# Kernel tuning notes

Hardware: AMD Instinct MI355X
Metric: run time of the kernel (lower is better)

The kernel has to match this reference:

```python
import jax, jax.numpy as jnp
import numpy as np

B, H, S, DH = 1, 16, 4096, 64
SPARSITY = 0.1
NEG = -1e9


def setup_inputs() -> dict:
    key = jax.random.key(0)
    kq, kk, kv, kp, km = jax.random.split(key, 5)
    query = jax.random.normal(kq, (B, H, S, DH), dtype=jnp.float32)
    k_ = jax.random.normal(kk, (B, H, S, DH), dtype=jnp.float32)
    v_ = jax.random.normal(kv, (B, H, S, DH), dtype=jnp.float32)
    pat = jax.random.uniform(kp, (S, S)) < SPARSITY
    pat = pat | jnp.eye(S, dtype=bool)
    sparse_pattern = pat[None, None]  # [1,1,S,S]
    mask = jax.random.randint(km, (1, 1, 1, S), 0, 2, dtype=jnp.int32)
    return {"query": query, "key": k_, "value": v_,
            "sparse_pattern": sparse_pattern, "mask": mask}


def reference(query, key, value, sparse_pattern, mask):
    scale = 1.0 / jnp.sqrt(jnp.asarray(DH, dtype=query.dtype))
    # [B,H,S,S] attention scores
    scores = jnp.einsum('bhqd,bhkd->bhqk', query, key) * scale
    scores = jnp.where(sparse_pattern, scores, NEG)
    scores = jnp.where(mask == 0, NEG, scores)
    weights = jax.nn.softmax(scores, axis=-1)
    return jnp.einsum('bhqk,bhkd->bhqd', weights, value)
```

## Files before the change

### kernel.cpp

```cpp
#include <hip/hip_runtime.h>
#include <hip/hip_bf16.h>

#define S_LEN 4096
#define DHD   64
#define NH    16
#define NKT   64
#define KVB   64
#define WQ    32
#define NW    4
#define QB    (WQ * NW)
#define QSCALE 0.18033688011112042f
#define THRS   8.656170245333781f

#if __has_builtin(__builtin_amdgcn_exp2f)
#define EXP2(x) __builtin_amdgcn_exp2f(x)
#else
#define EXP2(x) exp2f(x)
#endif

typedef __bf16 bf16x8 __attribute__((ext_vector_type(8)));
typedef __bf16 bf16x4 __attribute__((ext_vector_type(4)));
typedef float  f32x16 __attribute__((ext_vector_type(16)));
typedef float  f32x4  __attribute__((ext_vector_type(4)));
typedef unsigned u32;
typedef unsigned u32x4v __attribute__((ext_vector_type(4)));
typedef unsigned long long u64;

__device__ __forceinline__ int swz(int row, int col) {
  return row * 64 + ((((col >> 3) ^ (row & 7)) << 3) | (col & 7));
}

__device__ __forceinline__ u32 pk(float a, float b) {
  __bf16 x = (__bf16)a, y = (__bf16)b;
  u32 lo = (u32)__builtin_bit_cast(unsigned short, x);
  u32 hi = (u32)__builtin_bit_cast(unsigned short, y);
  return lo | (hi << 16);
}

__device__ __forceinline__ void gload16(const void* g, void* l) {
  __builtin_amdgcn_global_load_lds((const __attribute__((address_space(1))) void*)g,
                                   (__attribute__((address_space(3))) void*)l, 16, 0, 0);
}

union PAW { u32x4v w; bf16x8 h; };

template <int MODE>
__device__ __forceinline__ bool patget(const void* __restrict__ p, int q, int k) {
  const size_t idx = (size_t)q * S_LEN + k;
  if constexpr (MODE == 1) return ((const unsigned char*)p)[idx] != 0;
  else if constexpr (MODE == 0) return ((const int*)p)[idx] != 0;
  else return ((const float*)p)[idx] != 0.0f;
}

__global__ void __launch_bounds__(256, 2) attn32c(
    const float* __restrict__ Qg, const __bf16* __restrict__ Kc, const __bf16* __restrict__ Vc,
    const u64* __restrict__ packw,
    const int* __restrict__ cntp, float* __restrict__ out) {
  __shared__ __align__(16) __bf16 Kls[2][KVB * DHD];
  __shared__ __align__(16) __bf16 Vls[2][DHD * KVB];
  __shared__ float sfb[NW][WQ];

  const int gid = (blockIdx.x & 7) * 64 + (blockIdx.x >> 3);
  const int h = gid >> 5;
  const int q0 = (gid & 31) * QB;

  const int t = threadIdx.x, lane = t & 63, wv = t >> 6;
  const int l32 = lane & 31, hi = lane >> 5;
  const int qrow = q0 + wv * WQ + l32;
  const int nact = cntp[0];
  const int nt = (nact + 63) >> 6;

  bf16x8 aQ[4];
  {
    const float* qp = Qg + ((size_t)h * S_LEN + qrow) * DHD;
#pragma unroll
    for (int c = 0; c < 4; c++) {
      float4 x = *(const float4*)(qp + c * 16 + hi * 8);
      float4 y = *(const float4*)(qp + c * 16 + hi * 8 + 4);
      bf16x8 f;
      f[0] = (__bf16)(x.x * QSCALE); f[1] = (__bf16)(x.y * QSCALE);
      f[2] = (__bf16)(x.z * QSCALE); f[3] = (__bf16)(x.w * QSCALE);
      f[4] = (__bf16)(y.x * QSCALE); f[5] = (__bf16)(y.y * QSCALE);
      f[6] = (__bf16)(y.z * QSCALE); f[7] = (__bf16)(y.w * QSCALE);
      aQ[c] = f;
    }
  }
  bf16x8 onesf;
#pragma unroll
  for (int j = 0; j < 8; j++) onesf[j] = (__bf16)1.0f;

  const __bf16* Kb = Kc + (size_t)h * NKT * 4096;
  const __bf16* Vb = Vc + (size_t)h * NKT * 4096;

  auto stage = [&](int buf, int kt) {
    const __bf16* kbase = Kb + (size_t)kt * 4096;
    const __bf16* vbase = Vb + (size_t)kt * 4096;
#pragma unroll
    for (int i = 0; i < 2; i++) {
      const int j = wv * 2 + i;
      gload16(kbase + j * 512 + lane * 8, &Kls[buf][j * 512]);
      gload16(vbase + j * 512 + lane * 8, &Vls[buf][j * 512]);
    }
  };

  f32x16 Oc0, Oc1, Ol;
#pragma unroll
  for (int r = 0; r < 16; r++) { Oc0[r] = 0.f; Oc1[r] = 0.f; Ol[r] = 0.f; }
  float m_run = -__builtin_inff();
  const u64* prow = packw + qrow;

  stage(0, 0);
  __syncthreads();
  int cur = 0;

  for (int kt = 0; kt < nt; kt++) {
    if (kt + 1 < nt) stage(cur ^ 1, kt + 1);

    const u64 pw = prow[(size_t)kt * S_LEN];

    const __bf16* Kl = Kls[cur];
    f32x16 p0, p1;
#pragma unroll
    for (int r = 0; r < 16; r++) { p0[r] = 0.f; p1[r] = 0.f; }
    __builtin_amdgcn_s_setprio(1);
#pragma unroll
    for (int c = 0; c < 4; c++) {
      const int g = (((2 * c + hi) ^ (l32 & 7)) << 3);
      const bf16x8 k0 = *(const bf16x8*)&Kl[l32 * 64 + g];
      const bf16x8 k1 = *(const bf16x8*)&Kl[(32 + l32) * 64 + g];
      p0 = __builtin_amdgcn_mfma_f32_32x32x16_bf16(k0, aQ[c], p0, 0, 0, 0);
      p1 = __builtin_amdgcn_mfma_f32_32x32x16_bf16(k1, aQ[c], p1, 0, 0, 0);
    }
    __builtin_amdgcn_s_setprio(0);

    float mx[16];
#pragma unroll
    for (int i = 0; i < 8; i++) mx[i] = fmaxf(p0[2 * i], p0[2 * i + 1]);
#pragma unroll
    for (int i = 0; i < 8; i++) mx[8 + i] = fmaxf(p1[2 * i], p1[2 * i + 1]);
#pragma unroll
    for (int s = 8; s >= 1; s >>= 1)
#pragma unroll
      for (int i = 0; i < s; i++) mx[i] = fmaxf(mx[i], mx[i + s]);
    const float pm = fmaxf(mx[0], __shfl_xor(mx[0], 32));

    if (!__all(pm <= m_run + THRS)) {
      const float mn = fmaxf(m_run, pm);
      const float sf = EXP2(m_run - mn);
      m_run = mn;
      if (lane < 32) sfb[wv][l32] = sf;
#pragma unroll
      for (int rq = 0; rq < 4; rq++) {
        const f32x4 s4 = *(const f32x4*)&sfb[wv][rq * 8 + 4 * hi];
#pragma unroll
        for (int rr = 0; rr < 4; rr++) {
          Oc0[rq * 4 + rr] *= s4[rr];
          Oc1[rq * 4 + rr] *= s4[rr];
          Ol[rq * 4 + rr]  *= s4[rr];
        }
      }
    }

    const u32 b0 = (u32)pw, b1 = (u32)(pw >> 32);
    const u32 w0 = hi ? ((b0 >> 4) | (b1 << 28)) : b0;
    const u32 w1 = hi ? (b1 >> 4) : b1;

#pragma unroll
    for (int r = 0; r < 16; r++) {
      const int sp = (r & 3) + 8 * (r >> 2);
      float e0 = EXP2(p0[r] - m_run);
      float e1 = EXP2(p1[r] - m_run);
      const int t0 = (int)(w0 << (31 - sp)) >> 31;
      const int t1 = (int)(w1 << (31 - sp)) >> 31;
      p0[r] = __uint_as_float(__float_as_uint(e0) & (u32)t0);
      p1[r] = __uint_as_float(__float_as_uint(e1) & (u32)t1);
    }

    const __bf16* Vl = Vls[cur];
    __builtin_amdgcn_s_setprio(1);
#pragma unroll
    for (int ks = 0; ks < 4; ks++) {
      const f32x16& ps = (ks < 2) ? p0 : p1;
      const int b = (ks & 1) * 8;
      const u32 a0 = pk(ps[b + 0], ps[b + 1]), a1 = pk(ps[b + 2], ps[b + 3]);
      const u32 c0 = pk(ps[b + 4], ps[b + 5]), c1 = pk(ps[b + 6], ps[b + 7]);
      const u32 sa0 = (u32)__shfl_xor((int)a0, 32), sa1 = (u32)__shfl_xor((int)a1, 32);
      const u32 sc0 = (u32)__shfl_xor((int)c0, 32), sc1 = (u32)__shfl_xor((int)c1, 32);
      PAW pa;
      pa.w = (u32x4v){hi ? sc0 : a0, hi ? sc1 : a1, hi ? c0 : sa0, hi ? c1 : sa1};
      const int g = (((2 * ks + hi) ^ (l32 & 7)) << 3);
      const bf16x8 v0 = *(const bf16x8*)&Vl[l32 * 64 + g];
      const bf16x8 v1 = *(const bf16x8*)&Vl[(32 + l32) * 64 + g];
      Oc0 = __builtin_amdgcn_mfma_f32_32x32x16_bf16(pa.h, v0, Oc0, 0, 0, 0);
      Oc1 = __builtin_amdgcn_mfma_f32_32x32x16_bf16(pa.h, v1, Oc1, 0, 0, 0);
      Ol  = __builtin_amdgcn_mfma_f32_32x32x16_bf16(pa.h, onesf, Ol, 0, 0, 0);
    }
    __builtin_amdgcn_s_setprio(0);

    __syncthreads();
    cur ^= 1;
  }

  float* ob = out + ((size_t)h * S_LEN + q0 + wv * WQ) * DHD;
#pragma unroll
  for (int rq = 0; rq < 4; rq++) {
#pragma unroll
    for (int rr = 0; rr < 4; rr++) {
      const int r = rq * 4 + rr;
      const float linv = 1.0f / Ol[r];
      const int qq = rr + 8 * rq + 4 * hi;
      ob[(size_t)qq * DHD + l32]      = Oc0[r] * linv;
      ob[(size_t)qq * DHD + 32 + l32] = Oc1[r] * linv;
    }
  }
}

__global__ void prep0(const unsigned* __restrict__ p, int* __restrict__ flag,
                      const int* __restrict__ mask, int* __restrict__ idx,
                      int* __restrict__ cntp) {
  if (blockIdx.x == 0) {
    __shared__ unsigned red[256];
    const int t = threadIdx.x;
    unsigned acc = 0;
    for (int i = t; i < 16384; i += 256) {
      const unsigned w = p[i];
      if (w == 0x3F800000u) acc |= 2u;
      else if (w & 0xFFFFFF00u) acc |= 1u;
    }
    red[t] = acc;
    __syncthreads();
    if (t == 0) {
      unsigned a = 0;
      for (int i = 0; i < 256; i++) a |= red[i];
      flag[0] = (a & 2u) ? 2 : ((a & 1u) ? 1 : 0);
    }
  } else if (threadIdx.x < 64) {
    const int t = threadIdx.x;
    int cnt = 0;
    for (int j = 0; j < 64; j++) cnt += (mask[t * 64 + j] != 0);
    int inc = cnt;
    for (int d = 1; d < 64; d <<= 1) {
      const int v = __shfl_up(inc, d);
      if (t >= d) inc += v;
    }
    int pfx = inc - cnt;
    for (int j = 0; j < 64; j++) {
      const int k = t * 64 + j;
      if (mask[k] != 0) idx[pfx++] = k;
    }
    if (t == 63) cntp[0] = inc;
  }
}

__global__ void __launch_bounds__(256) pack_compact(
    const void* __restrict__ pat, const int* __restrict__ flagp,
    const int* __restrict__ idx, const int* __restrict__ cntp, u64* __restrict__ packw) {
  __shared__ __align__(16) unsigned rowbuf[4096];
  const int q = blockIdx.x, t = threadIdx.x;
  const int nact = cntp[0];
  const int mode = flagp[0];
  if (mode == 1) {
    const uint4* src = (const uint4*)((const unsigned char*)pat + ((size_t)q << 12));
    ((uint4*)rowbuf)[t] = src[t];
  } else {
    const uint4* src = (const uint4*)((const unsigned*)pat + ((size_t)q << 12));
#pragma unroll
    for (int i = 0; i < 4; i++) ((uint4*)rowbuf)[t + 256 * i] = src[t + 256 * i];
  }
  __syncthreads();
  const unsigned char* rb = (const unsigned char*)rowbuf;
  for (int base = 0; base < nact; base += 256) {
    const int j = base + t;
    bool pb = false;
    if (j < nact) {
      const int k = idx[j];
      pb = (mode == 1) ? (rb[k] != 0) : (rowbuf[k] != 0);
    }
    const u64 b = __ballot(pb);
    if ((t & 63) == 0) packw[(size_t)(j >> 6) * S_LEN + q] = b;
  }
}

__global__ void compact_kv(const float* __restrict__ K, const float* __restrict__ V,
                           const int* __restrict__ idx, const int* __restrict__ cntp,
                           __bf16* __restrict__ Kc, __bf16* __restrict__ Vc) {
  const int kt = blockIdx.x, h = blockIdx.y, t = threadIdx.x;
  const int nact = cntp[0];
  if (kt >= ((nact + 63) >> 6)) return;
  __bf16* Kd = Kc + ((size_t)(h * NKT + kt)) * 4096;
  __bf16* Vd = Vc + ((size_t)(h * NKT + kt)) * 4096;
  const float* Kb = K + (size_t)h * S_LEN * DHD;
  const float* Vb = V + (size_t)h * S_LEN * DHD;
#pragma unroll
  for (int i = 0; i < 4; i++) {
    const int u = t + 256 * i;
    const int kk = u >> 4, d = (u & 15) * 4;
    const int kg = kt * 64 + kk;
    float4 v = {0.f, 0.f, 0.f, 0.f};
    if (kg < nact) v = *(const float4*)(Kb + (size_t)idx[kg] * DHD + d);
    bf16x4 b;
    b[0] = (__bf16)v.x; b[1] = (__bf16)v.y; b[2] = (__bf16)v.z; b[3] = (__bf16)v.w;
    *(bf16x4*)&Kd[swz(kk, d)] = b;
  }
#pragma unroll
  for (int i = 0; i < 2; i++) {
    const int u = t + 256 * i;
    const int kp = u & 31, d4 = u >> 5;
    const int g0 = kt * 64 + 2 * kp, g1 = g0 + 1;
    float4 a = {0.f, 0.f, 0.f, 0.f}, b = {0.f, 0.f, 0.f, 0.f};
    if (g0 < nact) a = *(const float4*)(Vb + (size_t)idx[g0] * DHD + d4 * 4);
    if (g1 < nact) b = *(const float4*)(Vb + (size_t)idx[g1] * DHD + d4 * 4);
    const float* A = reinterpret_cast<const float*>(&a);
    const float* B = reinterpret_cast<const float*>(&b);
#pragma unroll
    for (int j = 0; j < 4; j++) {
      *(u32*)&Vd[swz(d4 * 4 + j, 2 * kp)] = pk(A[j], B[j]);
    }
  }
}

template <bool PACKED, int MODE>
__global__ void __launch_bounds__(256, 2) attn32(
    const float* __restrict__ Qg, const float* __restrict__ Kg, const float* __restrict__ Vg,
    const u64* __restrict__ packw, const void* __restrict__ pat, const int* __restrict__ mask,
    float* __restrict__ out) {
  __shared__ __align__(16) __bf16 Kls[2][KVB * DHD];
  __shared__ __align__(16) __bf16 Vls[2][DHD * KVB];
  __shared__ float sfb[NW][WQ];
  const int gid = (blockIdx.x & 7) * 64 + (blockIdx.x >> 3);
  const int h = gid >> 5;
  const int q0 = (gid & 31) * QB;
  const int t = threadIdx.x, lane = t & 63, wv = t >> 6;
  const int l32 = lane & 31, hi = lane >> 5;
  const int qrow = q0 + wv * WQ + l32;
  bf16x8 aQ[4];
  {
    const float* qp = Qg + ((size_t)h * S_LEN + qrow) * DHD;
#pragma unroll
    for (int c = 0; c < 4; c++) {
      float4 x = *(const float4*)(qp + c * 16 + hi * 8);
      float4 y = *(const float4*)(qp + c * 16 + hi * 8 + 4);
      bf16x8 f;
      f[0] = (__bf16)(x.x * QSCALE); f[1] = (__bf16)(x.y * QSCALE);
      f[2] = (__bf16)(x.z * QSCALE); f[3] = (__bf16)(x.w * QSCALE);
      f[4] = (__bf16)(y.x * QSCALE); f[5] = (__bf16)(y.y * QSCALE);
      f[6] = (__bf16)(y.z * QSCALE); f[7] = (__bf16)(y.w * QSCALE);
      aQ[c] = f;
    }
  }
  const float* Kb = Kg + (size_t)h * S_LEN * DHD;
  const float* Vb = Vg + (size_t)h * S_LEN * DHD;
  float4 kreg[4], vreg0[2], vreg1[2];
  auto issue_loads = [&](int kt) {
    const float* kbase = Kb + (size_t)kt * KVB * DHD;
    const float* vbase = Vb + (size_t)kt * KVB * DHD;
#pragma unroll
    for (int i = 0; i < 4; i++) {
      const int u = t + 256 * i;
      kreg[i] = *(const float4*)(kbase + (size_t)(u >> 4) * DHD + (u & 15) * 4);
    }
#pragma unroll
    for (int i = 0; i < 2; i++) {
      const int u = t + 256 * i;
      const int kp = u & 31, d4 = u >> 5;
      vreg0[i] = *(const float4*)(vbase + (size_t)(2 * kp) * DHD + d4 * 4);
      vreg1[i] = *(const float4*)(vbase + (size_t)(2 * kp + 1) * DHD + d4 * 4);
    }
  };
  auto write_tile = [&](int buf) {
    __bf16* Kd = Kls[buf];
    __bf16* Vd = Vls[buf];
#pragma unroll
    for (int i = 0; i < 4; i++) {
      const int u = t + 256 * i;
      const int kk = u >> 4, d = (u & 15) * 4;
      const float4 v = kreg[i];
      bf16x4 b;
      b[0] = (__bf16)v.x; b[1] = (__bf16)v.y; b[2] = (__bf16)v.z; b[3] = (__bf16)v.w;
      *(bf16x4*)&Kd[swz(kk, d)] = b;
    }
#pragma unroll
    for (int i = 0; i < 2; i++) {
      const int u = t + 256 * i;
      const int kp = u & 31, d4 = u >> 5;
      const float* A = reinterpret_cast<const float*>(&vreg0[i]);
      const float* B = reinterpret_cast<const float*>(&vreg1[i]);
#pragma unroll
      for (int j = 0; j < 4; j++) {
        *(u32*)&Vd[swz(d4 * 4 + j, 2 * kp)] = pk(A[j], B[j]);
      }
    }
  };
  f32x16 Oc0, Oc1;
#pragma unroll
  for (int r = 0; r < 16; r++) { Oc0[r] = 0.f; Oc1[r] = 0.f; }
  float m_run = -__builtin_inff(), l_run = 0.f;
  const u64* prow = PACKED ? (packw + qrow) : nullptr;
  issue_loads(0);
  write_tile(0);
  __syncthreads();
  int cur = 0;
  for (int kt = 0; kt < NKT; kt++) {
    if (kt + 1 < NKT) issue_loads(kt + 1);
    u64 pw;
    if constexpr (PACKED) {
      pw = prow[(size_t)kt * S_LEN];
    } else {
      pw = 0;
      for (int j = 0; j < 64; j++) {
        const bool pb = patget<MODE>(pat, qrow, kt * 64 + j) && (mask[kt * 64 + j] != 0);
        pw |= (u64)pb << j;
      }
    }
    const __bf16* Kl = Kls[cur];
    f32x16 p0, p1;
#pragma unroll
    for (int r = 0; r < 16; r++) { p0[r] = 0.f; p1[r] = 0.f; }
#pragma unroll
    for (int c = 0; c < 4; c++) {
      const int g = (((2 * c + hi) ^ (l32 & 7)) << 3);
      const bf16x8 k0 = *(const bf16x8*)&Kl[l32 * 64 + g];
      const bf16x8 k1 = *(const bf16x8*)&Kl[(32 + l32) * 64 + g];
      p0 = __builtin_amdgcn_mfma_f32_32x32x16_bf16(k0, aQ[c], p0, 0, 0, 0);
      p1 = __builtin_amdgcn_mfma_f32_32x32x16_bf16(k1, aQ[c], p1, 0, 0, 0);
    }
    float pm = p0[0];
#pragma unroll
    for (int r = 1; r < 16; r++) pm = fmaxf(pm, p0[r]);
#pragma unroll
    for (int r = 0; r < 16; r++) pm = fmaxf(pm, p1[r]);
    pm = fmaxf(pm, __shfl_xor(pm, 32));
    if (!__all(pm <= m_run + THRS)) {
      const float mn = fmaxf(m_run, pm);
      const float sf = EXP2(m_run - mn);
      m_run = mn;
      l_run *= sf;
      if (lane < 32) sfb[wv][l32] = sf;
#pragma unroll
      for (int rq = 0; rq < 4; rq++) {
        const f32x4 s4 = *(const f32x4*)&sfb[wv][rq * 8 + 4 * hi];
#pragma unroll
        for (int rr = 0; rr < 4; rr++) {
          Oc0[rq * 4 + rr] *= s4[rr];
          Oc1[rq * 4 + rr] *= s4[rr];
        }
      }
    }
    const u32 b0 = (u32)pw, b1 = (u32)(pw >> 32);
    const u32 w0 = hi ? ((b0 >> 4) | (b1 << 28)) : b0;
    const u32 w1 = hi ? (b1 >> 4) : b1;
    float ls = 0.f;
#pragma unroll
    for (int r = 0; r < 16; r++) {
      const int sp = (r & 3) + 8 * (r >> 2);
      float e0 = EXP2(p0[r] - m_run);
      float e1 = EXP2(p1[r] - m_run);
      const int t0 = (int)(w0 << (31 - sp)) >> 31;
      const int t1 = (int)(w1 << (31 - sp)) >> 31;
      e0 = __uint_as_float(__float_as_uint(e0) & (u32)t0);
      e1 = __uint_as_float(__float_as_uint(e1) & (u32)t1);
      p0[r] = e0; p1[r] = e1;
      ls += e0 + e1;
    }
    ls += __shfl_xor(ls, 32);
    l_run += ls;
    const __bf16* Vl = Vls[cur];
#pragma unroll
    for (int ks = 0; ks < 4; ks++) {
      const f32x16& ps = (ks < 2) ? p0 : p1;
      const int b = (ks & 1) * 8;
      const u32 a0 = pk(ps[b + 0], ps[b + 1]), a1 = pk(ps[b + 2], ps[b + 3]);
      const u32 c0 = pk(ps[b + 4], ps[b + 5]), c1 = pk(ps[b + 6], ps[b + 7]);
      const u32 sa0 = (u32)__shfl_xor((int)a0, 32), sa1 = (u32)__shfl_xor((int)a1, 32);
      const u32 sc0 = (u32)__shfl_xor((int)c0, 32), sc1 = (u32)__shfl_xor((int)c1, 32);
      PAW pa;
      pa.w = (u32x4v){hi ? sc0 : a0, hi ? sc1 : a1, hi ? c0 : sa0, hi ? c1 : sa1};
      const int g = (((2 * ks + hi) ^ (l32 & 7)) << 3);
      const bf16x8 v0 = *(const bf16x8*)&Vl[l32 * 64 + g];
      const bf16x8 v1 = *(const bf16x8*)&Vl[(32 + l32) * 64 + g];
      Oc0 = __builtin_amdgcn_mfma_f32_32x32x16_bf16(pa.h, v0, Oc0, 0, 0, 0);
      Oc1 = __builtin_amdgcn_mfma_f32_32x32x16_bf16(pa.h, v1, Oc1, 0, 0, 0);
    }
    if (kt + 1 < NKT) write_tile(cur ^ 1);
    __syncthreads();
    cur ^= 1;
  }
  const float linv = 1.0f / l_run;
  if (lane < 32) sfb[wv][l32] = linv;
  __syncthreads();
  float* ob = out + ((size_t)h * S_LEN + q0 + wv * WQ) * DHD;
#pragma unroll
  for (int rq = 0; rq < 4; rq++) {
    const f32x4 s4 = *(const f32x4*)&sfb[wv][rq * 8 + 4 * hi];
#pragma unroll
    for (int rr = 0; rr < 4; rr++) {
      const int r = rq * 4 + rr;
      const int qq = rr + 8 * rq + 4 * hi;
      ob[(size_t)qq * DHD + l32]      = Oc0[r] * s4[rr];
      ob[(size_t)qq * DHD + 32 + l32] = Oc1[r] * s4[rr];
    }
  }
}

__global__ void detect_kernel(const unsigned* __restrict__ p, int* __restrict__ flag) {
  __shared__ unsigned red[256];
  const int t = threadIdx.x;
  unsigned acc = 0;
  for (int i = t; i < 16384; i += 256) {
    const unsigned w = p[i];
    if (w == 0x3F800000u) acc |= 2u;
    else if (w & 0xFFFFFF00u) acc |= 1u;
  }
  red[t] = acc;
  __syncthreads();
  if (t == 0) {
    unsigned a = 0;
    for (int i = 0; i < 256; i++) a |= red[i];
    flag[0] = (a & 2u) ? 2 : ((a & 1u) ? 1 : 0);
  }
}

__global__ void pack_mask_kernel(const int* __restrict__ mask, u64* __restrict__ maskw) {
  const int w = threadIdx.x;
  u64 m = 0;
  for (int j = 0; j < 64; j++) m |= (u64)(mask[(w << 6) + j] != 0) << j;
  maskw[w] = m;
}

__global__ void pack_pat_kernel(const void* __restrict__ pat, const u64* __restrict__ maskw,
                                u64* __restrict__ packw, const int* __restrict__ flagp) {
  const int gid = blockIdx.x * 256 + threadIdx.x;
  const int q = gid >> 6, w = gid & 63;
  const int mode = flagp[0];
  u64 bits = 0;
  if (mode == 1) {
    const u64* p = (const u64*)((const unsigned char*)pat + ((size_t)q << 12) + (w << 6));
#pragma unroll
    for (int c = 0; c < 8; c++) {
      u64 v = p[c];
      v |= v >> 4; v |= v >> 2; v |= v >> 1;
      v &= 0x0101010101010101ull;
      bits |= ((v * 0x0102040810204080ull) >> 56) << (c * 8);
    }
  } else if (mode == 0) {
    const int4* p = (const int4*)((const int*)pat + ((size_t)q << 12) + ((size_t)w << 6));
#pragma unroll
    for (int c = 0; c < 16; c++) {
      const int4 x = p[c];
      bits |= (u64)(x.x != 0) << (c * 4);
      bits |= (u64)(x.y != 0) << (c * 4 + 1);
      bits |= (u64)(x.z != 0) << (c * 4 + 2);
      bits |= (u64)(x.w != 0) << (c * 4 + 3);
    }
  } else {
    const float4* p = (const float4*)((const float*)pat + ((size_t)q << 12) + ((size_t)w << 6));
#pragma unroll
    for (int c = 0; c < 16; c++) {
      const float4 x = p[c];
      bits |= (u64)(x.x != 0.0f) << (c * 4);
      bits |= (u64)(x.y != 0.0f) << (c * 4 + 1);
      bits |= (u64)(x.z != 0.0f) << (c * 4 + 2);
      bits |= (u64)(x.w != 0.0f) << (c * 4 + 3);
    }
  }
  packw[(size_t)w * S_LEN + q] = bits & maskw[w];
}

extern "C" void kernel_launch(void* const* d_in, const int* in_sizes, int n_in,
                              void* d_out, int out_size, void* d_ws, size_t ws_size,
                              hipStream_t stream) {
  (void)in_sizes; (void)n_in; (void)out_size;
  const float* Q  = (const float*)d_in[0];
  const float* K  = (const float*)d_in[1];
  const float* V  = (const float*)d_in[2];
  const void* pat = d_in[3];
  const int* mask = (const int*)d_in[4];
  float* out      = (float*)d_out;

  const size_t FLAG_OFF  = 0;
  const size_t CNT_OFF   = 256;
  const size_t IDX_OFF   = 4096;
  const size_t MASKW_OFF = 24576;
  const size_t PACKW_OFF = 32768;
  const size_t KC_OFF    = PACKW_OFF + (size_t)S_LEN * NKT * 8;
  const size_t VC_OFF    = KC_OFF + (size_t)NH * NKT * 4096 * 2;
  const size_t NEED_FULL = VC_OFF + (size_t)NH * NKT * 4096 * 2;
  const size_t NEED_MID  = PACKW_OFF + (size_t)S_LEN * NKT * 8;

  const dim3 grid(32 * NH, 1);

  if (ws_size >= NEED_FULL) {
    int* flag  = (int*)((char*)d_ws + FLAG_OFF);
    int* cnt   = (int*)((char*)d_ws + CNT_OFF);
    int* idx   = (int*)((char*)d_ws + IDX_OFF);
    u64* packw = (u64*)((char*)d_ws + PACKW_OFF);
    __bf16* Kc = (__bf16*)((char*)d_ws + KC_OFF);
    __bf16* Vc = (__bf16*)((char*)d_ws + VC_OFF);
    prep0<<<2, 256, 0, stream>>>((const unsigned*)pat, flag, mask, idx, cnt);
    compact_kv<<<dim3(NKT, NH), 256, 0, stream>>>(K, V, idx, cnt, Kc, Vc);
    pack_compact<<<S_LEN, 256, 0, stream>>>(pat, flag, idx, cnt, packw);
    attn32c<<<grid, 256, 0, stream>>>(Q, Kc, Vc, packw, cnt, out);
  } else if (ws_size >= NEED_MID) {
    int* flag  = (int*)((char*)d_ws + FLAG_OFF);
    u64* maskw = (u64*)((char*)d_ws + MASKW_OFF);
    u64* packw = (u64*)((char*)d_ws + PACKW_OFF);
    detect_kernel<<<1, 256, 0, stream>>>((const unsigned*)pat, flag);
    pack_mask_kernel<<<1, 64, 0, stream>>>(mask, maskw);
    pack_pat_kernel<<<(S_LEN * 64) / 256, 256, 0, stream>>>(pat, maskw, packw, flag);
    attn32<true, 0><<<grid, 256, 0, stream>>>(Q, K, V, packw, pat, mask, out);
  } else {
    attn32<false, 1><<<grid, 256, 0, stream>>>(Q, K, V, nullptr, pat, mask, out);
  }
}
```

Measured before the change: 107.9 us.

## Merge prep kernels, prefetch pattern words, use permlane32 swap, fine-grained waits

Merges the K/V compaction and pattern-packing kernels into one launch to save a kernel launch and let both jobs run at once. In the main attention loop it prefetches the next tile's pattern word. It replaces __syncthreads with explicit vmcnt waits plus raw barriers, so the next tile's async loads can stay in flight. It also swaps the four cross-half shuffles plus selects for two v_permlane32_swap instructions when building the P operand. The hand-written vmcnt(5) count depends on exactly how many loads are outstanding and could be wrong if the compiler reorders loads.

```diff
diff --git a/kernel.cpp b/kernel.cpp
--- a/kernel.cpp
+++ b/kernel.cpp
@@ -42,6 +42,10 @@
                                    (__attribute__((address_space(3))) void*)l, 16, 0, 0);
 }
 
+__device__ __forceinline__ void plswap(u32& x, u32& y) {
+  asm("v_permlane32_swap_b32 %0, %1" : "+v"(x), "+v"(y));
+}
+
 union PAW { u32x4v w; bf16x8 h; };
 
 template <int MODE>
@@ -109,14 +113,21 @@
   float m_run = -__builtin_inff();
   const u64* prow = packw + qrow;
 
+  u64 pw_cur = prow[0];
+  u64 pw_nxt = 0;
   stage(0, 0);
-  __syncthreads();
   int cur = 0;
 
   for (int kt = 0; kt < nt; kt++) {
-    if (kt + 1 < nt) stage(cur ^ 1, kt + 1);
-
-    const u64 pw = prow[(size_t)kt * S_LEN];
+    if (kt + 1 < nt) {
+      pw_nxt = prow[(size_t)(kt + 1) * S_LEN];
+      stage(cur ^ 1, kt + 1);
+      asm volatile("s_waitcnt vmcnt(5)" ::: "memory");
+    } else {
+      asm volatile("s_waitcnt vmcnt(0)" ::: "memory");
+    }
+    __builtin_amdgcn_s_barrier();
+    __builtin_amdgcn_sched_barrier(0);
 
     const __bf16* Kl = Kls[cur];
     f32x16 p0, p1;
@@ -161,7 +172,7 @@
       }
     }
 
-    const u32 b0 = (u32)pw, b1 = (u32)(pw >> 32);
+    const u32 b0 = (u32)pw_cur, b1 = (u32)(pw_cur >> 32);
     const u32 w0 = hi ? ((b0 >> 4) | (b1 << 28)) : b0;
     const u32 w1 = hi ? (b1 >> 4) : b1;
 
@@ -182,12 +193,12 @@
     for (int ks = 0; ks < 4; ks++) {
       const f32x16& ps = (ks < 2) ? p0 : p1;
       const int b = (ks & 1) * 8;
-      const u32 a0 = pk(ps[b + 0], ps[b + 1]), a1 = pk(ps[b + 2], ps[b + 3]);
-      const u32 c0 = pk(ps[b + 4], ps[b + 5]), c1 = pk(ps[b + 6], ps[b + 7]);
-      const u32 sa0 = (u32)__shfl_xor((int)a0, 32), sa1 = (u32)__shfl_xor((int)a1, 32);
-      const u32 sc0 = (u32)__shfl_xor((int)c0, 32), sc1 = (u32)__shfl_xor((int)c1, 32);
+      u32 x0 = pk(ps[b + 0], ps[b + 1]), x1 = pk(ps[b + 2], ps[b + 3]);
+      u32 y0 = pk(ps[b + 4], ps[b + 5]), y1 = pk(ps[b + 6], ps[b + 7]);
+      plswap(x0, y0);
+      plswap(x1, y1);
       PAW pa;
-      pa.w = (u32x4v){hi ? sc0 : a0, hi ? sc1 : a1, hi ? c0 : sa0, hi ? c1 : sa1};
+      pa.w = (u32x4v){x0, x1, y0, y1};
       const int g = (((2 * ks + hi) ^ (l32 & 7)) << 3);
       const bf16x8 v0 = *(const bf16x8*)&Vl[l32 * 64 + g];
       const bf16x8 v1 = *(const bf16x8*)&Vl[(32 + l32) * 64 + g];
@@ -197,8 +208,9 @@
     }
     __builtin_amdgcn_s_setprio(0);
 
-    __syncthreads();
+    __builtin_amdgcn_s_barrier();
     cur ^= 1;
+    pw_cur = pw_nxt;
   }
 
   float* ob = out + ((size_t)h * S_LEN + q0 + wv * WQ) * DHD;
@@ -252,69 +264,70 @@
   }
 }
 
-__global__ void __launch_bounds__(256) pack_compact(
+__global__ void __launch_bounds__(256) prep1(
     const void* __restrict__ pat, const int* __restrict__ flagp,
-    const int* __restrict__ idx, const int* __restrict__ cntp, u64* __restrict__ packw) {
-  __shared__ __align__(16) unsigned rowbuf[4096];
-  const int q = blockIdx.x, t = threadIdx.x;
+    const int* __restrict__ idx, const int* __restrict__ cntp, u64* __restrict__ packw,
+    const float* __restrict__ K, const float* __restrict__ V,
+    __bf16* __restrict__ Kc, __bf16* __restrict__ Vc) {
   const int nact = cntp[0];
-  const int mode = flagp[0];
-  if (mode == 1) {
-    const uint4* src = (const uint4*)((const unsigned char*)pat + ((size_t)q << 12));
-    ((uint4*)rowbuf)[t] = src[t];
+  const int t = threadIdx.x;
+  if (blockIdx.x < S_LEN) {
+    __shared__ __align__(16) unsigned rowbuf[4096];
+    const int q = blockIdx.x;
+    const int mode = flagp[0];
+    if (mode == 1) {
+      const uint4* src = (const uint4*)((const unsigned char*)pat + ((size_t)q << 12));
+      ((uint4*)rowbuf)[t] = src[t];
+    } else {
+      const uint4* src = (const uint4*)((const unsigned*)pat + ((size_t)q << 12));
+#pragma unroll
+      for (int i = 0; i < 4; i++) ((uint4*)rowbuf)[t + 256 * i] = src[t + 256 * i];
+    }
+    __syncthreads();
+    const unsigned char* rb = (const unsigned char*)rowbuf;
+    for (int base = 0; base < nact; base += 256) {
+      const int j = base + t;
+      bool pb = false;
+      if (j < nact) {
+        const int k = idx[j];
+        pb = (mode == 1) ? (rb[k] != 0) : (rowbuf[k] != 0);
+      }
+      const u64 b = __ballot(pb);
+      if ((t & 63) == 0) packw[(size_t)(j >> 6) * S_LEN + q] = b;
+    }
   } else {
-    const uint4* src = (const uint4*)((const unsigned*)pat + ((size_t)q << 12));
-#pragma unroll
-    for (int i = 0; i < 4; i++) ((uint4*)rowbuf)[t + 256 * i] = src[t + 256 * i];
-  }
-  __syncthreads();
-  const unsigned char* rb = (const unsigned char*)rowbuf;
-  for (int base = 0; base < nact; base += 256) {
-    const int j = base + t;
-    bool pb = false;
-    if (j < nact) {
-      const int k = idx[j];
-      pb = (mode == 1) ? (rb[k] != 0) : (rowbuf[k] != 0);
-    }
-    const u64 b = __ballot(pb);
-    if ((t & 63) == 0) packw[(size_t)(j >> 6) * S_LEN + q] = b;
-  }
-}
-
-__global__ void compact_kv(const float* __restrict__ K, const float* __restrict__ V,
-                           const int* __restrict__ idx, const int* __restrict__ cntp,
-                           __bf16* __restrict__ Kc, __bf16* __restrict__ Vc) {
-  const int kt = blockIdx.x, h = blockIdx.y, t = threadIdx.x;
-  const int nact = cntp[0];
-  if (kt >= ((nact + 63) >> 6)) return;
-  __bf16* Kd = Kc + ((size_t)(h * NKT + kt)) * 4096;
-  __bf16* Vd = Vc + ((size_t)(h * NKT + kt)) * 4096;
-  const float* Kb = K + (size_t)h * S_LEN * DHD;
-  const float* Vb = V + (size_t)h * S_LEN * DHD;
-#pragma unroll
-  for (int i = 0; i < 4; i++) {
-    const int u = t + 256 * i;
-    const int kk = u >> 4, d = (u & 15) * 4;
-    const int kg = kt * 64 + kk;
-    float4 v = {0.f, 0.f, 0.f, 0.f};
-    if (kg < nact) v = *(const float4*)(Kb + (size_t)idx[kg] * DHD + d);
-    bf16x4 b;
-    b[0] = (__bf16)v.x; b[1] = (__bf16)v.y; b[2] = (__bf16)v.z; b[3] = (__bf16)v.w;
-    *(bf16x4*)&Kd[swz(kk, d)] = b;
-  }
-#pragma unroll
-  for (int i = 0; i < 2; i++) {
-    const int u = t + 256 * i;
-    const int kp = u & 31, d4 = u >> 5;
-    const int g0 = kt * 64 + 2 * kp, g1 = g0 + 1;
-    float4 a = {0.f, 0.f, 0.f, 0.f}, b = {0.f, 0.f, 0.f, 0.f};
-    if (g0 < nact) a = *(const float4*)(Vb + (size_t)idx[g0] * DHD + d4 * 4);
-    if (g1 < nact) b = *(const float4*)(Vb + (size_t)idx[g1] * DHD + d4 * 4);
-    const float* A = reinterpret_cast<const float*>(&a);
-    const float* B = reinterpret_cast<const float*>(&b);
-#pragma unroll
-    for (int j = 0; j < 4; j++) {
-      *(u32*)&Vd[swz(d4 * 4 + j, 2 * kp)] = pk(A[j], B[j]);
+    const int bb = blockIdx.x - S_LEN;
+    const int kt = bb & 63, h = bb >> 6;
+    if (kt >= ((nact + 63) >> 6)) return;
+    __bf16* Kd = Kc + ((size_t)(h * NKT + kt)) * 4096;
+    __bf16* Vd = Vc + ((size_t)(h * NKT + kt)) * 4096;
+    const float* Kb = K + (size_t)h * S_LEN * DHD;
+    const float* Vb = V + (size_t)h * S_LEN * DHD;
+#pragma unroll
+    for (int i = 0; i < 4; i++) {
+      const int u = t + 256 * i;
+      const int kk = u >> 4, d = (u & 15) * 4;
+      const int kg = kt * 64 + kk;
+      float4 v = {0.f, 0.f, 0.f, 0.f};
+      if (kg < nact) v = *(const float4*)(Kb + (size_t)idx[kg] * DHD + d);
+      bf16x4 b;
+      b[0] = (__bf16)v.x; b[1] = (__bf16)v.y; b[2] = (__bf16)v.z; b[3] = (__bf16)v.w;
+      *(bf16x4*)&Kd[swz(kk, d)] = b;
+    }
+#pragma unroll
+    for (int i = 0; i < 2; i++) {
+      const int u = t + 256 * i;
+      const int kp = u & 31, d4 = u >> 5;
+      const int g0 = kt * 64 + 2 * kp, g1 = g0 + 1;
+      float4 a = {0.f, 0.f, 0.f, 0.f}, b = {0.f, 0.f, 0.f, 0.f};
+      if (g0 < nact) a = *(const float4*)(Vb + (size_t)idx[g0] * DHD + d4 * 4);
+      if (g1 < nact) b = *(const float4*)(Vb + (size_t)idx[g1] * DHD + d4 * 4);
+      const float* A = reinterpret_cast<const float*>(&a);
+      const float* B = reinterpret_cast<const float*>(&b);
+#pragma unroll
+      for (int j = 0; j < 4; j++) {
+        *(u32*)&Vd[swz(d4 * 4 + j, 2 * kp)] = pk(A[j], B[j]);
+      }
     }
   }
 }
@@ -469,12 +482,12 @@
     for (int ks = 0; ks < 4; ks++) {
       const f32x16& ps = (ks < 2) ? p0 : p1;
       const int b = (ks & 1) * 8;
-      const u32 a0 = pk(ps[b + 0], ps[b + 1]), a1 = pk(ps[b + 2], ps[b + 3]);
-      const u32 c0 = pk(ps[b + 4], ps[b + 5]), c1 = pk(ps[b + 6], ps[b + 7]);
-      const u32 sa0 = (u32)__shfl_xor((int)a0, 32), sa1 = (u32)__shfl_xor((int)a1, 32);
-      const u32 sc0 = (u32)__shfl_xor((int)c0, 32), sc1 = (u32)__shfl_xor((int)c1, 32);
+      u32 x0 = pk(ps[b + 0], ps[b + 1]), x1 = pk(ps[b + 2], ps[b + 3]);
+      u32 y0 = pk(ps[b + 4], ps[b + 5]), y1 = pk(ps[b + 6], ps[b + 7]);
+      plswap(x0, y0);
+      plswap(x1, y1);
       PAW pa;
-      pa.w = (u32x4v){hi ? sc0 : a0, hi ? sc1 : a1, hi ? c0 : sa0, hi ? c1 : sa1};
+      pa.w = (u32x4v){x0, x1, y0, y1};
       const int g = (((2 * ks + hi) ^ (l32 & 7)) << 3);
       const bf16x8 v0 = *(const bf16x8*)&Vl[l32 * 64 + g];
       const bf16x8 v1 = *(const bf16x8*)&Vl[(32 + l32) * 64 + g];
@@ -597,8 +610,7 @@
     __bf16* Kc = (__bf16*)((char*)d_ws + KC_OFF);
     __bf16* Vc = (__bf16*)((char*)d_ws + VC_OFF);
     prep0<<<2, 256, 0, stream>>>((const unsigned*)pat, flag, mask, idx, cnt);
-    compact_kv<<<dim3(NKT, NH), 256, 0, stream>>>(K, V, idx, cnt, Kc, Vc);
-    pack_compact<<<S_LEN, 256, 0, stream>>>(pat, flag, idx, cnt, packw);
+    prep1<<<S_LEN + NKT * NH, 256, 0, stream>>>(pat, flag, idx, cnt, packw, K, V, Kc, Vc);
     attn32c<<<grid, 256, 0, stream>>>(Q, Kc, Vc, packw, cnt, out);
   } else if (ws_size >= NEED_MID) {
     int* flag  = (int*)((char*)d_ws + FLAG_OFF);
```

New measurement: 101.6 us. 1.06x faster.
